# Performance work log

Hardware: AMD Instinct MI355X
Metric: run time of the kernel (lower is better)

Reference implementation:

```python
import jax, jax.numpy as jnp
import numpy as np

N, E, D = 50000, 800000, 256   # nodes, edges, hidden_dim
H, B, A = 8, 4, 3              # num_heads, num_bases, num_aggregators (symnorm,sum,max)
F = D // H                      # per-head width = bases feature width
G = 64                          # number of graphs in the batch
EPS = 1e-5                      # GraphNorm eps


def setup_inputs() -> dict:
    key = jax.random.key(0)
    ks = jax.random.split(key, 8)
    glorot = lambda k, shape: jax.random.normal(k, shape, jnp.float32) * np.sqrt(2.0 / (shape[0] + shape[1])).astype(np.float32)
    return {
        "node": jax.random.normal(ks[0], (N, D), jnp.float32),
        "edge_attr": jax.random.normal(ks[1], (E, 1), jnp.float32),  # unused by layer, kept for signature fidelity
        "W_bases": glorot(ks[2], (D, B * F)),                 # EGConv bases linear (no bias)
        "W_comb": glorot(ks[3], (D, H * B * A)),              # EGConv combination-weight linear
        "b_comb": jnp.zeros((H * B * A,), jnp.float32),
        "conv_bias": jnp.zeros((D,), jnp.float32),
        "gn_weight": jnp.ones((D,), jnp.float32),             # GraphNorm gamma
        "gn_bias": jnp.zeros((D,), jnp.float32),              # GraphNorm beta
        "gn_mean_scale": jnp.ones((D,), jnp.float32),         # GraphNorm alpha
        "edge_index": jax.random.randint(ks[4], (2, E), 0, N, dtype=jnp.int32),
        "batch": jnp.sort(jax.random.randint(ks[5], (N,), 0, G, dtype=jnp.int32)),
    }


def _forward(node, W_bases, W_comb, b_comb, conv_bias, gn_weight, gn_bias, gn_mean_scale, edge_index, batch):
    n = node.shape[0]
    loops = jnp.arange(n, dtype=edge_index.dtype)
    src = jnp.concatenate([edge_index[0], loops])  # add self-loops (EGConv add_self_loops=True / gcn_norm)
    dst = jnp.concatenate([edge_index[1], loops])

    # gcn_norm symmetric weights deg^-1/2[src] * deg^-1/2[dst]
    deg = jax.ops.segment_sum(jnp.ones_like(src, dtype=node.dtype), dst, num_segments=n)
    dinv = jnp.where(deg > 0, jax.lax.rsqrt(deg), 0.0)
    sym_w = dinv[src] * dinv[dst]

    bases = node @ W_bases            # [N, B*F]
    comb = node @ W_comb + b_comb     # [N, H*B*A]

    msg = bases[src]                  # [E+N, B*F] edge gather (dominant traffic)
    agg_sym = jax.ops.segment_sum(msg * sym_w[:, None], dst, num_segments=n)
    agg_sum = jax.ops.segment_sum(msg, dst, num_segments=n)
    agg_max = jax.ops.segment_max(msg, dst, num_segments=n)  # self-loops guarantee non-empty segments

    aggregated = jnp.stack([agg_sym, agg_sum, agg_max], axis=1)       # [N, A, B*F]
    aggregated = aggregated.reshape(n, A * B, F)                      # (a,b) fused index, as in PyG view
    weightings = comb.reshape(n, H, B * A)
    h = jnp.einsum('nhk,nkf->nhf', weightings, aggregated).reshape(n, D) + conv_bias

    # GraphNorm: per-graph mean/var with learnable mean scale alpha
    counts = jnp.maximum(jax.ops.segment_sum(jnp.ones((n,), node.dtype), batch, num_segments=G), 1.0)
    mean = jax.ops.segment_sum(h, batch, num_segments=G) / counts[:, None]
    hc = h - gn_mean_scale * mean[batch]
    var = jax.ops.segment_sum(hc * hc, batch, num_segments=G) / counts[:, None]
    out = gn_weight * hc * jax.lax.rsqrt(var[batch] + EPS) + gn_bias
    return jax.nn.relu(out)


def reference(node, edge_attr, W_bases, W_comb, b_comb, conv_bias, gn_weight, gn_bias, gn_mean_scale, edge_index, batch):
    del edge_attr  # unused by EGConv_layer, present in the torch forward signature
    return _forward(node, W_bases, W_comb, b_comb, conv_bias, gn_weight, gn_bias, gn_mean_scale, edge_index, batch)
```

## Files before the change

kernel.cpp:

```cpp
#include <hip/hip_runtime.h>
#include <hip/hip_bf16.h>

#define NN 50000
#define EE 800000
#define DD 256
#define BF 128
#define HC 96
#define GG 64
#define NT 14
#define KCN 8
#define NB 49
#define RS 12500
#define RC 4
#define CS 12500
#define CC 64
#define SL 8

typedef short s16x8 __attribute__((ext_vector_type(8)));
typedef float f32x4 __attribute__((ext_vector_type(4)));

static __device__ __forceinline__ float b2f(unsigned u) {
    unsigned x = u << 16;
    float f;
    __builtin_memcpy(&f, &x, 4);
    return f;
}
static __device__ __forceinline__ unsigned short f2b(float f) {
    unsigned x;
    __builtin_memcpy(&x, &f, 4);
    unsigned lsb = (x >> 16) & 1u;
    x += 0x7fffu + lsb;
    return (unsigned short)(x >> 16);
}
static __device__ __forceinline__ unsigned pack_trunc(float lo, float hi) {
    unsigned ulo, uhi;
    __builtin_memcpy(&ulo, &lo, 4);
    __builtin_memcpy(&uhi, &hi, 4);
    return (ulo >> 16) | (uhi & 0xffff0000u);
}

__global__ void k_setup(const unsigned short* node_u16, int* flag,
                        const void* bcomb, const void* cbias, const void* gw,
                        const void* gb, const void* gms,
                        float* bcombF, float* cbiasF, float* gwF, float* gbF, float* gmsF,
                        const int* batch, int* goff) {
    if (blockIdx.x == 0) {
        __shared__ int cnt;
        if (threadIdx.x == 0) cnt = 0;
        __syncthreads();
        int local = 0;
        #pragma unroll
        for (int j = 0; j < 4; j++) {
            int idx = 2 * (threadIdx.x * 4 + j);
            unsigned short u = node_u16[idx];
            int e = (u >> 7) & 0xFF;
            if (e < 100 || e > 140) local++;
        }
        atomicAdd(&cnt, local);
        __syncthreads();
        int isf = (cnt > 256) ? 1 : 0;
        if (threadIdx.x == 0) flag[0] = isf;
        int d = threadIdx.x;
        auto rd = [&](const void* p, int i) -> float {
            return isf ? ((const float*)p)[i] : b2f(((const unsigned short*)p)[i]);
        };
        if (d < HC) bcombF[d] = rd(bcomb, d);
        cbiasF[d] = rd(cbias, d);
        gwF[d] = rd(gw, d);
        gbF[d] = rd(gb, d);
        gmsF[d] = rd(gms, d);
    } else {
        int g = threadIdx.x;
        if (g > GG) return;
        int lo = 0, hi = NN;
        while (lo < hi) { int mid = (lo + hi) >> 1; if (batch[mid] < g) lo = mid + 1; else hi = mid; }
        goff[g] = lo;
    }
}

__global__ __launch_bounds__(256) void k_ehist(const int* ei, int* partial) {
    __shared__ int hist[RS];
    int c = blockIdx.x, r = blockIdx.y;
    for (int i = threadIdx.x; i < RS; i += 256) hist[i] = 0;
    __syncthreads();
    int base = r * RS;
    const int* dstp = ei + EE + (size_t)c * CS;
    for (int i = threadIdx.x; i < CS; i += 256) {
        int d = dstp[i] - base;
        if ((unsigned)d < RS) atomicAdd(&hist[d], 1);
    }
    __syncthreads();
    int* o = partial + (size_t)c * NN + base;
    for (int i = threadIdx.x; i < RS; i += 256) o[i] = hist[i];
}

__global__ void k_colscan(int* partial, int* deg) {
    int n = blockIdx.x * 256 + threadIdx.x;
    if (n >= NN) return;
    int run = 0;
    for (int c = 0; c < CC; c++) {
        size_t idx = (size_t)c * NN + n;
        int v = partial[idx];
        partial[idx] = run;
        run += v;
    }
    deg[n] = run + 1;
}

__global__ void k_scan1(const int* deg, int* bsum) {
    __shared__ int lds[256];
    int b = blockIdx.x, t = threadIdx.x;
    int base = b * 1024 + t * 4;
    int s = 0;
    #pragma unroll
    for (int j = 0; j < 4; j++) { int idx = base + j; if (idx < NN) s += deg[idx]; }
    lds[t] = s; __syncthreads();
    for (int ofs = 128; ofs > 0; ofs >>= 1) {
        if (t < ofs) lds[t] += lds[t + ofs];
        __syncthreads();
    }
    if (t == 0) bsum[b] = lds[0];
}

__global__ void k_scan2(const int* bsum, int* bpre, int* row_off) {
    if (threadIdx.x == 0) {
        int r = 0;
        for (int i = 0; i < NB; i++) { bpre[i] = r; r += bsum[i]; }
        row_off[NN] = r;
    }
}

__global__ void k_scan3(const int* deg, const int* bpre, int* row_off, float* dinv, int* csr) {
    __shared__ int lds[256];
    int b = blockIdx.x, t = threadIdx.x;
    int base = b * 1024 + t * 4;
    int d[4]; int s = 0;
    #pragma unroll
    for (int j = 0; j < 4; j++) { int idx = base + j; d[j] = (idx < NN) ? deg[idx] : 0; s += d[j]; }
    lds[t] = s; __syncthreads();
    for (int ofs = 1; ofs < 256; ofs <<= 1) {
        int add = (t >= ofs) ? lds[t - ofs] : 0;
        __syncthreads();
        lds[t] += add;
        __syncthreads();
    }
    int excl = lds[t] - s + bpre[b];
    #pragma unroll
    for (int j = 0; j < 4; j++) {
        int idx = base + j;
        if (idx < NN) {
            row_off[idx] = excl;
            csr[excl] = idx;
            excl += d[j];
            dinv[idx] = rsqrtf((float)deg[idx]);
        }
    }
}

__global__ __launch_bounds__(256) void k_escatter(const int* ei, const int* row_off,
                                                  const int* partial, int* csr) {
    __shared__ int cur[RS];
    int c = blockIdx.x, r = blockIdx.y;
    int base = r * RS;
    const int* po = partial + (size_t)c * NN + base;
    const int* ro = row_off + base;
    for (int i = threadIdx.x; i < RS; i += 256) cur[i] = ro[i] + 1 + po[i];
    __syncthreads();
    const int* srcp = ei + (size_t)c * CS;
    const int* dstp = ei + EE + (size_t)c * CS;
    for (int i = threadIdx.x; i < CS; i += 256) {
        int d = dstp[i] - base;
        if ((unsigned)d < RS) {
            int slot = atomicAdd(&cur[d], 1);
            csr[slot] = srcp[i];
        }
    }
}

__global__ void k_pack(const int* flag, const void* Wb, const void* Wc, unsigned short* wpack) {
    int t = blockIdx.x, kc = blockIdx.y, lane = threadIdx.x;
    int isf = flag[0];
    int n = t * 16 + (lane & 15);
    int kb = kc * 32 + (lane >> 4) * 8;
    unsigned short* o = wpack + (size_t)(((t * KCN) + kc) * 64 + lane) * 8;
    #pragma unroll
    for (int j = 0; j < 8; j++) {
        int k = kb + j;
        int src = (n < BF) ? (k * BF + n) : (k * HC + (n - BF));
        const void* W = (n < BF) ? Wb : Wc;
        o[j] = isf ? f2b(((const float*)W)[src]) : ((const unsigned short*)W)[src];
    }
}

__global__ __launch_bounds__(256) void k_gemm(const int* flag, const void* node,
                                              const unsigned short* wpack, const float* bcombF,
                                              unsigned short* bases, float* comb) {
    int wv = threadIdx.x >> 6, lane = threadIdx.x & 63;
    int row0 = blockIdx.x * 64 + wv * 16;
    int m = row0 + (lane & 15);
    int mc = m < NN ? m : NN - 1;
    int kg = lane >> 4;
    int isf = flag[0];
    const s16x8* bp = reinterpret_cast<const s16x8*>(wpack);
    f32x4 acc[NT];
    #pragma unroll
    for (int t = 0; t < NT; t++) acc[t] = (f32x4){0.f, 0.f, 0.f, 0.f};
    if (isf) {
        const float* nf = (const float*)node + (size_t)mc * DD;
        for (int kc = 0; kc < KCN; kc++) {
            const f32x4* src = reinterpret_cast<const f32x4*>(nf + kc * 32 + kg * 8);
            f32x4 x0 = src[0], x1 = src[1];
            union { s16x8 v; unsigned u[4]; } a;
            a.u[0] = pack_trunc(x0[0], x0[1]);
            a.u[1] = pack_trunc(x0[2], x0[3]);
            a.u[2] = pack_trunc(x1[0], x1[1]);
            a.u[3] = pack_trunc(x1[2], x1[3]);
            #pragma unroll
            for (int t = 0; t < NT; t++) {
                s16x8 b = bp[(size_t)(t * KCN + kc) * 64 + lane];
                acc[t] = __builtin_amdgcn_mfma_f32_16x16x32_bf16(a.v, b, acc[t], 0, 0, 0);
            }
        }
    } else {
        const s16x8* ap = reinterpret_cast<const s16x8*>(node);
        for (int kc = 0; kc < KCN; kc++) {
            s16x8 a = ap[(size_t)mc * 32 + kc * 4 + kg];
            #pragma unroll
            for (int t = 0; t < NT; t++) {
                s16x8 b = bp[(size_t)(t * KCN + kc) * 64 + lane];
                acc[t] = __builtin_amdgcn_mfma_f32_16x16x32_bf16(a, b, acc[t], 0, 0, 0);
            }
        }
    }
    int colb = lane & 15;
    #pragma unroll
    for (int t = 0; t < NT; t++) {
        int nc = t * 16 + colb;
        #pragma unroll
        for (int i = 0; i < 4; i++) {
            int r = row0 + kg * 4 + i;
            if (r < NN) {
                float v = acc[t][i];
                if (nc < BF) bases[(size_t)r * BF + nc] = f2b(v);
                else comb[(size_t)r * HC + (nc - BF)] = v + bcombF[nc - BF];
            }
        }
    }
}

__global__ __launch_bounds__(256) void k_agg(const int* flag, const unsigned short* bases,
                                             const float* comb, const float* dinv,
                                             const int* row_off, const int* csr,
                                             const float* cbiasF, void* hout) {
    __shared__ float2 lds[4][3][64];
    int wv = threadIdx.x >> 6, lane = threadIdx.x & 63;
    int v = blockIdx.x * 4 + wv;
    int r0 = row_off[v], r1 = row_off[v + 1];
    float dv = dinv[v];
    const unsigned* bp = reinterpret_cast<const unsigned*>(bases);
    float sy0 = 0.f, sy1 = 0.f, su0 = 0.f, su1 = 0.f;
    float mx0 = -3.4e38f, mx1 = -3.4e38f;
    for (int base = r0; base < r1; base += 64) {
        int nload = r1 - base; if (nload > 64) nload = 64;
        int sidx = 0; float wgt = 0.f;
        if (lane < nload) { sidx = csr[base + lane]; wgt = dinv[sidx] * dv; }
        int j = 0;
        for (; j + 4 <= nload; j += 4) {
            int s0 = __shfl(sidx, j),     s1 = __shfl(sidx, j + 1);
            int s2 = __shfl(sidx, j + 2), s3 = __shfl(sidx, j + 3);
            float w0 = __shfl(wgt, j),     w1 = __shfl(wgt, j + 1);
            float w2 = __shfl(wgt, j + 2), w3 = __shfl(wgt, j + 3);
            unsigned g0 = bp[(size_t)s0 * 64 + lane];
            unsigned g1 = bp[(size_t)s1 * 64 + lane];
            unsigned g2 = bp[(size_t)s2 * 64 + lane];
            unsigned g3 = bp[(size_t)s3 * 64 + lane];
            float a, b;
            a = b2f(g0 & 0xffffu); b = b2f(g0 >> 16);
            sy0 += w0 * a; sy1 += w0 * b; su0 += a; su1 += b; mx0 = fmaxf(mx0, a); mx1 = fmaxf(mx1, b);
            a = b2f(g1 & 0xffffu); b = b2f(g1 >> 16);
            sy0 += w1 * a; sy1 += w1 * b; su0 += a; su1 += b; mx0 = fmaxf(mx0, a); mx1 = fmaxf(mx1, b);
            a = b2f(g2 & 0xffffu); b = b2f(g2 >> 16);
            sy0 += w2 * a; sy1 += w2 * b; su0 += a; su1 += b; mx0 = fmaxf(mx0, a); mx1 = fmaxf(mx1, b);
            a = b2f(g3 & 0xffffu); b = b2f(g3 >> 16);
            sy0 += w3 * a; sy1 += w3 * b; su0 += a; su1 += b; mx0 = fmaxf(mx0, a); mx1 = fmaxf(mx1, b);
        }
        for (; j < nload; j++) {
            int s0 = __shfl(sidx, j); float w0 = __shfl(wgt, j);
            unsigned g0 = bp[(size_t)s0 * 64 + lane];
            float a = b2f(g0 & 0xffffu), b = b2f(g0 >> 16);
            sy0 += w0 * a; sy1 += w0 * b; su0 += a; su1 += b; mx0 = fmaxf(mx0, a); mx1 = fmaxf(mx1, b);
        }
    }
    lds[wv][0][lane] = (float2){sy0, sy1};
    lds[wv][1][lane] = (float2){su0, su1};
    lds[wv][2][lane] = (float2){mx0, mx1};
    __syncthreads();
    const float* P0 = (const float*)&lds[wv][0][0];
    const float* P1 = (const float*)&lds[wv][1][0];
    const float* P2 = (const float*)&lds[wv][2][0];
    int d0 = lane * 4;
    int hh = d0 >> 5;
    float cb[12];
    #pragma unroll
    for (int k = 0; k < 12; k++) cb[k] = comb[(size_t)v * HC + hh * 12 + k];
    float y[4];
    #pragma unroll
    for (int i = 0; i < 4; i++) {
        int d = d0 + i, f = d & 31;
        float acc = cbiasF[d];
        #pragma unroll
        for (int k = 0; k < 12; k++) {
            int a = k >> 2, b = k & 3;
            const float* P = (a == 0) ? P0 : ((a == 1) ? P1 : P2);
            acc += cb[k] * P[b * 32 + f];
        }
        y[i] = acc;
    }
    if (flag[0]) {
        f32x4 o = {y[0], y[1], y[2], y[3]};
        reinterpret_cast<f32x4*>(hout)[(size_t)v * 64 + lane] = o;
    } else {
        union { unsigned short e[4]; uint2 u; } o;
        #pragma unroll
        for (int i = 0; i < 4; i++) o.e[i] = f2b(y[i]);
        reinterpret_cast<uint2*>(hout)[(size_t)v * 64 + lane] = o.u;
    }
}

__global__ void k_stats1(const int* flag, const void* h, const int* goff, float* sstat) {
    int g = blockIdx.x, s = blockIdx.y, t = threadIdx.x;
    int isf = flag[0];
    int v0 = goff[g], v1 = goff[g + 1];
    float sum = 0.f, sq = 0.f;
    if (isf) {
        const float* hf = (const float*)h;
        for (int v = v0 + s; v < v1; v += SL) {
            float x = hf[(size_t)v * DD + t];
            sum += x; sq += x * x;
        }
    } else {
        const unsigned short* hb = (const unsigned short*)h;
        for (int v = v0 + s; v < v1; v += SL) {
            float x = b2f(hb[(size_t)v * DD + t]);
            sum += x; sq += x * x;
        }
    }
    size_t o = ((size_t)(g * SL + s)) * (2 * DD);
    sstat[o + t] = sum;
    sstat[o + DD + t] = sq;
}

__global__ void k_stats2(const float* sstat, const int* goff,
                         const float* gwF, const float* gbF, const float* gmsF,
                         float* sA, float* sB) {
    int g = blockIdx.x, d = threadIdx.x;
    float sum = 0.f, sq = 0.f;
    #pragma unroll
    for (int s = 0; s < SL; s++) {
        size_t o = ((size_t)(g * SL + s)) * (2 * DD);
        sum += sstat[o + d];
        sq  += sstat[o + DD + d];
    }
    int c = goff[g + 1] - goff[g];
    float cnt = (float)(c > 1 ? c : 1);
    float mu = sum / cnt;
    float m2 = sq / cnt;
    float al = gmsF[d];
    float var = m2 - mu * mu * (2.f * al - al * al);
    float rstd = rsqrtf(var + 1e-5f);
    float sa = gwF[d] * rstd;
    sA[g * DD + d] = sa;
    sB[g * DD + d] = gbF[d] - sa * al * mu;
}

__global__ void k_out(const int* flag, const int* batch, const float* sA, const float* sB, void* out) {
    int tid = blockIdx.x * 256 + threadIdx.x;
    int v = tid >> 6, q = tid & 63;
    if (v >= NN) return;
    int g = batch[v];
    f32x4 a = reinterpret_cast<const f32x4*>(sA)[g * 64 + q];
    f32x4 b = reinterpret_cast<const f32x4*>(sB)[g * 64 + q];
    if (flag[0]) {
        f32x4 x = reinterpret_cast<const f32x4*>(out)[(size_t)v * 64 + q];
        f32x4 y;
        #pragma unroll
        for (int i = 0; i < 4; i++) y[i] = fmaxf(x[i] * a[i] + b[i], 0.f);
        reinterpret_cast<f32x4*>(out)[(size_t)v * 64 + q] = y;
    } else {
        uint2 xr = reinterpret_cast<const uint2*>(out)[(size_t)v * 64 + q];
        float x0 = b2f(xr.x & 0xffffu), x1 = b2f(xr.x >> 16);
        float x2 = b2f(xr.y & 0xffffu), x3 = b2f(xr.y >> 16);
        union { unsigned short e[4]; uint2 u; } o;
        o.e[0] = f2b(fmaxf(x0 * a[0] + b[0], 0.f));
        o.e[1] = f2b(fmaxf(x1 * a[1] + b[1], 0.f));
        o.e[2] = f2b(fmaxf(x2 * a[2] + b[2], 0.f));
        o.e[3] = f2b(fmaxf(x3 * a[3] + b[3], 0.f));
        reinterpret_cast<uint2*>(out)[(size_t)v * 64 + q] = o.u;
    }
}

extern "C" void kernel_launch(void* const* d_in, const int* in_sizes, int n_in,
                              void* d_out, int out_size, void* d_ws, size_t ws_size,
                              hipStream_t stream) {
    const void* node  = d_in[0];
    const void* Wb    = d_in[2];
    const void* Wc    = d_in[3];
    const void* bcomb = d_in[4];
    const void* cbias = d_in[5];
    const void* gw    = d_in[6];
    const void* gb    = d_in[7];
    const void* gms   = d_in[8];
    const int* ei     = (const int*)d_in[9];
    const int* batch  = (const int*)d_in[10];

    char* w = (char*)d_ws;
    size_t off = 0;
    auto alloc = [&](size_t bytes) -> void* {
        off = (off + 255) & ~(size_t)255;
        void* p = w + off;
        off += bytes;
        return p;
    };
    unsigned short* bases = (unsigned short*)alloc((size_t)NN * BF * 2);
    float* comb    = (float*)alloc((size_t)NN * HC * 4);
    int*   csr     = (int*)alloc((size_t)(EE + NN) * 4);
    int*   partial = (int*)alloc((size_t)CC * NN * 4);
    int*   deg     = (int*)alloc((size_t)NN * 4);
    float* dinv    = (float*)alloc((size_t)NN * 4);
    int*   row_off = (int*)alloc((size_t)(NN + 1) * 4);
    int*   bsum    = (int*)alloc((size_t)NB * 4);
    int*   bpre    = (int*)alloc((size_t)NB * 4);
    int*   goff    = (int*)alloc((size_t)(GG + 1) * 4);
    float* sstat   = (float*)alloc((size_t)GG * SL * 2 * DD * 4);
    float* sA      = (float*)alloc((size_t)GG * DD * 4);
    float* sB      = (float*)alloc((size_t)GG * DD * 4);
    unsigned short* wpack = (unsigned short*)alloc((size_t)NT * KCN * 64 * 8 * 2);
    int*   flag    = (int*)alloc(256);
    float* bcombF  = (float*)alloc(HC * 4);
    float* cbiasF  = (float*)alloc(DD * 4);
    float* gwF     = (float*)alloc(DD * 4);
    float* gbF     = (float*)alloc(DD * 4);
    float* gmsF    = (float*)alloc(DD * 4);

    k_setup<<<2, 256, 0, stream>>>((const unsigned short*)node, flag, bcomb, cbias, gw, gb, gms,
                                   bcombF, cbiasF, gwF, gbF, gmsF, batch, goff);
    k_ehist<<<dim3(CC, RC), 256, 0, stream>>>(ei, partial);
    k_colscan<<<(NN + 255) / 256, 256, 0, stream>>>(partial, deg);
    k_scan1<<<NB, 256, 0, stream>>>(deg, bsum);
    k_scan2<<<1, 64, 0, stream>>>(bsum, bpre, row_off);
    k_scan3<<<NB, 256, 0, stream>>>(deg, bpre, row_off, dinv, csr);
    k_escatter<<<dim3(CC, RC), 256, 0, stream>>>(ei, row_off, partial, csr);
    k_pack<<<dim3(NT, KCN), 64, 0, stream>>>(flag, Wb, Wc, wpack);
    k_gemm<<<(NN + 63) / 64, 256, 0, stream>>>(flag, node, wpack, bcombF, bases, comb);
    k_agg<<<NN / 4, 256, 0, stream>>>(flag, bases, comb, dinv, row_off, csr, cbiasF, d_out);
    k_stats1<<<dim3(GG, SL), 256, 0, stream>>>(flag, d_out, goff, sstat);
    k_stats2<<<GG, 256, 0, stream>>>(sstat, goff, gwF, gbF, gmsF, sA, sB);
    k_out<<<(NN * 64 + 255) / 256, 256, 0, stream>>>(flag, batch, sA, sB, d_out);
}
```

Baseline: 312.0 us.

## Store intermediate h as bf16 scratch and split CSR scatter into more row chunks

```diff
diff --git a/kernel.cpp b/kernel.cpp
--- a/kernel.cpp
+++ b/kernel.cpp
@@ -10,8 +10,8 @@
 #define NT 14
 #define KCN 8
 #define NB 49
-#define RS 12500
-#define RC 4
+#define RS 3125
+#define RC 16
 #define CS 12500
 #define CC 64
 #define SL 8
@@ -170,9 +170,10 @@
     const int* dstp = ei + EE + (size_t)c * CS;
     for (int i = threadIdx.x; i < CS; i += 256) {
         int d = dstp[i] - base;
+        int s = srcp[i];
         if ((unsigned)d < RS) {
             int slot = atomicAdd(&cur[d], 1);
-            csr[slot] = srcp[i];
+            csr[slot] = s;
         }
     }
 }
@@ -248,10 +249,10 @@
     }
 }
 
-__global__ __launch_bounds__(256) void k_agg(const int* flag, const unsigned short* bases,
+__global__ __launch_bounds__(256) void k_agg(const unsigned short* bases,
                                              const float* comb, const float* dinv,
                                              const int* row_off, const int* csr,
-                                             const float* cbiasF, void* hout) {
+                                             const float* cbiasF, unsigned short* h) {
     __shared__ float2 lds[4][3][64];
     int wv = threadIdx.x >> 6, lane = threadIdx.x & 63;
     int v = blockIdx.x * 4 + wv;
@@ -303,7 +304,7 @@
     float cb[12];
     #pragma unroll
     for (int k = 0; k < 12; k++) cb[k] = comb[(size_t)v * HC + hh * 12 + k];
-    float y[4];
+    union { unsigned short e[4]; uint2 u; } o;
     #pragma unroll
     for (int i = 0; i < 4; i++) {
         int d = d0 + i, f = d & 31;
@@ -314,36 +315,18 @@
             const float* P = (a == 0) ? P0 : ((a == 1) ? P1 : P2);
             acc += cb[k] * P[b * 32 + f];
         }
-        y[i] = acc;
-    }
-    if (flag[0]) {
-        f32x4 o = {y[0], y[1], y[2], y[3]};
-        reinterpret_cast<f32x4*>(hout)[(size_t)v * 64 + lane] = o;
-    } else {
-        union { unsigned short e[4]; uint2 u; } o;
-        #pragma unroll
-        for (int i = 0; i < 4; i++) o.e[i] = f2b(y[i]);
-        reinterpret_cast<uint2*>(hout)[(size_t)v * 64 + lane] = o.u;
-    }
-}
-
-__global__ void k_stats1(const int* flag, const void* h, const int* goff, float* sstat) {
+        o.e[i] = f2b(acc);
+    }
+    reinterpret_cast<uint2*>(h)[(size_t)v * 64 + lane] = o.u;
+}
+
+__global__ void k_stats1(const unsigned short* h, const int* goff, float* sstat) {
     int g = blockIdx.x, s = blockIdx.y, t = threadIdx.x;
-    int isf = flag[0];
     int v0 = goff[g], v1 = goff[g + 1];
     float sum = 0.f, sq = 0.f;
-    if (isf) {
-        const float* hf = (const float*)h;
-        for (int v = v0 + s; v < v1; v += SL) {
-            float x = hf[(size_t)v * DD + t];
-            sum += x; sq += x * x;
-        }
-    } else {
-        const unsigned short* hb = (const unsigned short*)h;
-        for (int v = v0 + s; v < v1; v += SL) {
-            float x = b2f(hb[(size_t)v * DD + t]);
-            sum += x; sq += x * x;
-        }
+    for (int v = v0 + s; v < v1; v += SL) {
+        float x = b2f(h[(size_t)v * DD + t]);
+        sum += x; sq += x * x;
     }
     size_t o = ((size_t)(g * SL + s)) * (2 * DD);
     sstat[o + t] = sum;
@@ -373,28 +356,27 @@
     sB[g * DD + d] = gbF[d] - sa * al * mu;
 }
 
-__global__ void k_out(const int* flag, const int* batch, const float* sA, const float* sB, void* out) {
+__global__ void k_out(const int* flag, const unsigned short* h, const int* batch,
+                      const float* sA, const float* sB, void* out) {
     int tid = blockIdx.x * 256 + threadIdx.x;
     int v = tid >> 6, q = tid & 63;
     if (v >= NN) return;
     int g = batch[v];
+    uint2 xr = reinterpret_cast<const uint2*>(h)[(size_t)v * 64 + q];
     f32x4 a = reinterpret_cast<const f32x4*>(sA)[g * 64 + q];
     f32x4 b = reinterpret_cast<const f32x4*>(sB)[g * 64 + q];
+    float x0 = b2f(xr.x & 0xffffu), x1 = b2f(xr.x >> 16);
+    float x2 = b2f(xr.y & 0xffffu), x3 = b2f(xr.y >> 16);
+    float y0 = fmaxf(x0 * a[0] + b[0], 0.f);
+    float y1 = fmaxf(x1 * a[1] + b[1], 0.f);
+    float y2 = fmaxf(x2 * a[2] + b[2], 0.f);
+    float y3 = fmaxf(x3 * a[3] + b[3], 0.f);
     if (flag[0]) {
-        f32x4 x = reinterpret_cast<const f32x4*>(out)[(size_t)v * 64 + q];
-        f32x4 y;
-        #pragma unroll
-        for (int i = 0; i < 4; i++) y[i] = fmaxf(x[i] * a[i] + b[i], 0.f);
+        f32x4 y = {y0, y1, y2, y3};
         reinterpret_cast<f32x4*>(out)[(size_t)v * 64 + q] = y;
     } else {
-        uint2 xr = reinterpret_cast<const uint2*>(out)[(size_t)v * 64 + q];
-        float x0 = b2f(xr.x & 0xffffu), x1 = b2f(xr.x >> 16);
-        float x2 = b2f(xr.y & 0xffffu), x3 = b2f(xr.y >> 16);
         union { unsigned short e[4]; uint2 u; } o;
-        o.e[0] = f2b(fmaxf(x0 * a[0] + b[0], 0.f));
-        o.e[1] = f2b(fmaxf(x1 * a[1] + b[1], 0.f));
-        o.e[2] = f2b(fmaxf(x2 * a[2] + b[2], 0.f));
-        o.e[3] = f2b(fmaxf(x3 * a[3] + b[3], 0.f));
+        o.e[0] = f2b(y0); o.e[1] = f2b(y1); o.e[2] = f2b(y2); o.e[3] = f2b(y3);
         reinterpret_cast<uint2*>(out)[(size_t)v * 64 + q] = o.u;
     }
 }
@@ -423,6 +405,7 @@
     };
     unsigned short* bases = (unsigned short*)alloc((size_t)NN * BF * 2);
     float* comb    = (float*)alloc((size_t)NN * HC * 4);
+    unsigned short* h = (unsigned short*)alloc((size_t)NN * DD * 2);
     int*   csr     = (int*)alloc((size_t)(EE + NN) * 4);
     int*   partial = (int*)alloc((size_t)CC * NN * 4);
     int*   deg     = (int*)alloc((size_t)NN * 4);
@@ -452,8 +435,8 @@
     k_escatter<<<dim3(CC, RC), 256, 0, stream>>>(ei, row_off, partial, csr);
     k_pack<<<dim3(NT, KCN), 64, 0, stream>>>(flag, Wb, Wc, wpack);
     k_gemm<<<(NN + 63) / 64, 256, 0, stream>>>(flag, node, wpack, bcombF, bases, comb);
-    k_agg<<<NN / 4, 256, 0, stream>>>(flag, bases, comb, dinv, row_off, csr, cbiasF, d_out);
-    k_stats1<<<dim3(GG, SL), 256, 0, stream>>>(flag, d_out, goff, sstat);
+    k_agg<<<NN / 4, 256, 0, stream>>>(bases, comb, dinv, row_off, csr, cbiasF, h);
+    k_stats1<<<dim3(GG, SL), 256, 0, stream>>>(h, goff, sstat);
     k_stats2<<<GG, 256, 0, stream>>>(sstat, goff, gwF, gbF, gmsF, sA, sB);
-    k_out<<<(NN * 64 + 255) / 256, 256, 0, stream>>>(flag, batch, sA, sB, d_out);
-}
+    k_out<<<(NN * 64 + 255) / 256, 256, 0, stream>>>(flag, h, batch, sA, sB, d_out);
+}
```

New measurement: 313.1 us. No clear change (+0.4%).
